# Optimization experiments

Hardware: AMD Instinct MI355X
Metric: run time of the kernel (lower is better)

Reference implementation:

```python
import jax, jax.numpy as jnp
import numpy as np
from jax import lax

MAX_LEN = 40
SOS_ID = 2
VOCAB, EMB, HID, CTX = 32000, 512, 1024, 64
H2 = HID // 2
B, S = 256, 128


def gru_cell(x, h, wih, whh, bih, bhh):
    # PyTorch GRU equations: gates ordered (r, z, n)
    gx = x @ wih.T + bih
    gh = h @ whh.T + bhh
    rx, zx, nx = jnp.split(gx, 3, axis=-1)
    rh, zh, nh = jnp.split(gh, 3, axis=-1)
    r = jax.nn.sigmoid(rx + rh)
    z = jax.nn.sigmoid(zx + zh)
    n = jnp.tanh(nx + r * nh)
    return (1.0 - z) * n + z * h


def setup_inputs() -> dict:
    key = jax.random.key(0)
    ks = jax.random.split(key, 16)
    sd = 0.02
    emb_table = jax.random.normal(ks[0], (VOCAB, EMB), jnp.float32) * sd
    emb_table = emb_table.at[0].set(0.0)  # padding_idx=0
    def w(k, shape):
        return jax.random.normal(k, shape, jnp.float32) * sd
    inp = {
        "input_ids": jax.random.randint(ks[1], (B, S), 0, VOCAB),
        "context_vec": jax.random.normal(ks[2], (B, CTX), jnp.float32),
        "emb_table": emb_table,
        # encoder fwd direction
        "enc_wih_f": w(ks[3], (3 * H2, EMB)),
        "enc_whh_f": w(ks[4], (3 * H2, H2)),
        "enc_bih_f": w(ks[5], (3 * H2,)),
        "enc_bhh_f": w(ks[6], (3 * H2,)),
        # encoder bwd direction
        "enc_wih_b": w(ks[7], (3 * H2, EMB)),
        "enc_whh_b": w(ks[8], (3 * H2, H2)),
        "enc_bih_b": w(ks[9], (3 * H2,)),
        "enc_bhh_b": w(ks[10], (3 * H2,)),
        # decoder GRU: input = emb + hidden + context
        "dec_wih": w(ks[11], (3 * HID, EMB + HID + CTX)),
        "dec_whh": w(ks[12], (3 * HID, HID)),
        "dec_bih": w(ks[13], (3 * HID,)),
        "dec_bhh": w(ks[14], (3 * HID,)),
        "wout": w(ks[15], (VOCAB, HID)),
        "bout": jnp.zeros((VOCAB,), jnp.float32),
    }
    return inp


def reference(input_ids, context_vec, emb_table,
              enc_wih_f, enc_whh_f, enc_bih_f, enc_bhh_f,
              enc_wih_b, enc_whh_b, enc_bih_b, enc_bhh_b,
              dec_wih, dec_whh, dec_bih, dec_bhh, wout, bout):
    b = input_ids.shape[0]
    emb = emb_table[input_ids]                      # [B,S,E]
    emb_t = jnp.swapaxes(emb, 0, 1)                 # [S,B,E]

    def enc_f(h, x):
        return gru_cell(x, h, enc_wih_f, enc_whh_f, enc_bih_f, enc_bhh_f), None

    def enc_b(h, x):
        return gru_cell(x, h, enc_wih_b, enc_whh_b, enc_bih_b, enc_bhh_b), None

    h0 = jnp.zeros((b, H2), emb.dtype)
    hf, _ = lax.scan(enc_f, h0, emb_t)
    hb, _ = lax.scan(enc_b, h0, emb_t[::-1])
    # replicate torch's h_n.view(batch, -1) on a (2,B,H2) tensor (contiguous reshape)
    encoder_ctx = jnp.stack([hf, hb], axis=0).reshape(b, HID)   # [B,HID]

    ctx = jnp.concatenate([encoder_ctx, context_vec], axis=-1)  # [B,HID+CTX]
    h_dec0 = jnp.zeros((b, HID), emb.dtype)
    prev0 = jnp.full((b,), SOS_ID, dtype=jnp.int32)

    def dec_step(carry, _):
        h, prev = carry
        x = jnp.concatenate([emb_table[prev], ctx], axis=-1)
        h = gru_cell(x, h, dec_wih, dec_whh, dec_bih, dec_bhh)
        logits = h @ wout.T + bout                  # [B,V]
        probs = jax.nn.softmax(logits, axis=-1)
        nxt = jnp.argmax(probs, axis=-1).astype(jnp.int32)
        sel = jnp.take_along_axis(probs, nxt[:, None], axis=1)[:, 0]
        lp = jnp.log(sel + 1e-12)
        return (h, nxt), (nxt, lp)

    (_, _), (toks, lps) = lax.scan(dec_step, (h_dec0, prev0), None, length=MAX_LEN)
    return toks.T, lps.T   # [B,MAX_LEN] tokens, [B,MAX_LEN] log-probs
```

## Files before the change

kernel.cpp:

```cpp
#include <hip/hip_runtime.h>
#include <hip/hip_bf16.h>
#include <math.h>

#define B_    256
#define S_    128
#define EMB_  512
#define H2_   512
#define HID_  1024
#define CTX_  64
#define VOC_  32000
#define TMAX_ 40
#define SOS_  2

typedef unsigned short u16;
typedef __attribute__((ext_vector_type(8))) short short8;
typedef __attribute__((ext_vector_type(4))) float f32x4;

__device__ __forceinline__ float4 ld4(const float* p) {
    return *reinterpret_cast<const float4*>(p);
}
__device__ __forceinline__ float sigmoidf_(float x) { return 1.f / (1.f + expf(-x)); }
__device__ __forceinline__ u16 f2bf(float x) {
    union { float f; unsigned int u; } v; v.f = x;
    unsigned int r = v.u + 0x7FFFu + ((v.u >> 16) & 1u);
    return (u16)(r >> 16);
}
__device__ __forceinline__ unsigned pk2(float a, float b) {
    float2 t; t.x = a; t.y = b;
    __hip_bfloat162 h = __float22bfloat162_rn(t);
    return *reinterpret_cast<unsigned*>(&h);
}
__device__ __forceinline__ void merge_top2(float& v1, int& i1, float& v2, int& i2,
                                           float ov1, int oi1, float ov2, int oi2)
{
    if (ov1 > v1 || (ov1 == v1 && oi1 < i1)) {
        float tv = v1; int ti = i1;
        v1 = ov1; i1 = oi1;
        if (ov2 > tv || (ov2 == tv && oi2 < ti)) { v2 = ov2; i2 = oi2; }
        else                                     { v2 = tv;  i2 = ti;  }
    } else {
        if (ov1 > v2 || (ov1 == v2 && oi1 < i2)) { v2 = ov1; i2 = oi1; }
    }
}

template<int BM, int BN, int TM, int TN, int AMODE, int BGATHER, int BIASM>
__launch_bounds__(256)
__global__ void gemm_nt(const float* __restrict__ Ap,
                        const int*   __restrict__ ids,
                        const float* __restrict__ Ex,
                        const float* __restrict__ Bp, int ldb, int bofs,
                        const float* __restrict__ bias,
                        const float* __restrict__ addsrc,
                        float* __restrict__ Cp, int ldc,
                        int lda, int K, int s_base, int sdir)
{
    constexpr int BK = 32;
    __shared__ float As[BK][BM + 4];
    __shared__ float Bs[BK][BN + 4];
    const int t  = threadIdx.x;
    const int tx = t & 15, ty = t >> 4;
    const int m_base = blockIdx.y * BM;
    const int n_base = blockIdx.x * BN;

    float acc[TM][TN];
#pragma unroll
    for (int i = 0; i < TM; ++i)
#pragma unroll
        for (int j = 0; j < TN; ++j) acc[i][j] = 0.f;

    constexpr int A_PER = BM * BK / 4 / 256;
    constexpr int B_PER = BN * BK / 4 / 256;

    for (int k0 = 0; k0 < K; k0 += BK) {
#pragma unroll
        for (int j = 0; j < A_PER; ++j) {
            int f   = t + j * 256;
            int row = f >> 3;
            int kk  = (f & 7) << 2;
            int m   = m_base + row;
            float4 v;
            if constexpr (AMODE == 0) {
                v = ld4(Ap + (size_t)m * lda + k0 + kk);
            } else if constexpr (AMODE == 3) {
                int id = ids[m];
                v = ld4(Ex + (size_t)id * EMB_ + k0 + kk);
            } else {
                int k = k0 + kk;
                if (k < HID_) v = ld4(Ap + (size_t)m * HID_ + k);
                else          v = ld4(Ex + (size_t)m * CTX_ + (k - HID_));
            }
            As[kk + 0][row] = v.x; As[kk + 1][row] = v.y;
            As[kk + 2][row] = v.z; As[kk + 3][row] = v.w;
        }
#pragma unroll
        for (int j = 0; j < B_PER; ++j) {
            int f   = t + j * 256;
            int row = f >> 3;
            int kk  = (f & 7) << 2;
            float4 v;
            if constexpr (BGATHER == 1) {
                int n = n_base + row;
                int s = n >> 8, b = n & 255;
                int id = ids[b * S_ + s_base + sdir * s];
                v = ld4(Ex + (size_t)id * EMB_ + k0 + kk);
            } else {
                v = ld4(Bp + (size_t)(n_base + row) * ldb + bofs + k0 + kk);
            }
            Bs[kk + 0][row] = v.x; Bs[kk + 1][row] = v.y;
            Bs[kk + 2][row] = v.z; Bs[kk + 3][row] = v.w;
        }
        __syncthreads();
#pragma unroll
        for (int kk = 0; kk < BK; ++kk) {
            float a[TM], b[TN];
            *(float4*)&a[0] = ld4(&As[kk][ty * TM]);
            if constexpr (TM == 8) *(float4*)&a[4] = ld4(&As[kk][ty * TM + 4]);
            *(float4*)&b[0] = ld4(&Bs[kk][tx * TN]);
            if constexpr (TN == 8) *(float4*)&b[4] = ld4(&Bs[kk][tx * TN + 4]);
#pragma unroll
            for (int i = 0; i < TM; ++i)
#pragma unroll
                for (int j = 0; j < TN; ++j) acc[i][j] += a[i] * b[j];
        }
        __syncthreads();
    }
#pragma unroll
    for (int i = 0; i < TM; ++i) {
        int m = m_base + ty * TM + i;
#pragma unroll
        for (int j = 0; j < TN; ++j) {
            int n = n_base + tx * TN + j;
            float v = acc[i][j];
            if (bias) v += BIASM ? bias[m] : bias[n];
            if (addsrc) v += addsrc[(size_t)m * ldc + n];
            Cp[(size_t)m * ldc + n] = v;
        }
    }
}

__global__ void whh_trans(const float* __restrict__ whh_f, const float* __restrict__ whh_b,
                          float* __restrict__ whhU_f, float* __restrict__ whhU_b)
{
    int idx = blockIdx.x * 256 + threadIdx.x;
    const float* src = blockIdx.y ? whh_b : whh_f;
    float*       dst = blockIdx.y ? whhU_b : whhU_f;
    int k  = idx / 1536;
    int rem = idx - k * 1536;
    int g  = rem >> 9;
    int u  = rem & 511;
    dst[idx] = src[(size_t)(g * 512 + u) * 512 + k];
}

__global__ void wbf_conv(const float* __restrict__ wout, unsigned* __restrict__ wbf, int npairs)
{
    int idx = blockIdx.x * 256 + threadIdx.x;
    if (idx >= npairs) return;
    float2 v = *reinterpret_cast<const float2*>(wout + (size_t)idx * 2);
    wbf[idx] = pk2(v.x, v.y);
}

union EncSM {
    struct { float hbuf[2][512][4]; } rec;
    struct { float As[32][132]; float Bs[32][132]; } gx;
};

__launch_bounds__(512)
__global__ void enc_fused(const float* __restrict__ grec_f, const float* __restrict__ grec_b,
                          float* __restrict__ gout_f, float* __restrict__ gout_b,
                          const float* __restrict__ whhU_f, const float* __restrict__ whhU_b,
                          const float* __restrict__ bhh_f, const float* __restrict__ bhh_b,
                          const float* __restrict__ wih_f, const float* __restrict__ wih_b,
                          const float* __restrict__ bih_f, const float* __restrict__ bih_b,
                          const int* __restrict__ ids, const float* __restrict__ emb,
                          float* __restrict__ hT, int do_rec, int gx_chunk, int nsteps)
{
    __shared__ __align__(16) EncSM sm;
    const int t = threadIdx.x;
    const int idx = blockIdx.x;
    const int grp = idx & 15;

    if (grp >= 8) {
        if (gx_chunk < 0) return;
        const int g = (idx >> 4) * 8 + (grp - 8);
        const int dz  = g >= 192;
        const int t192 = dz ? g - 192 : g;
        const int m_base = (t192 & 15) * 128;
        const int n_base = (t192 >> 4) * 128;
        const float* W    = dz ? wih_b : wih_f;
        const float* bias = dz ? bih_b : bih_f;
        float*       Cp   = dz ? gout_b : gout_f;
        const int s_base  = dz ? (127 - 8 * gx_chunk) : (8 * gx_chunk);
        const int sdir    = dz ? -1 : 1;
        const int tx = t & 31, ty = t >> 5;

        float acc[8][4];
#pragma unroll
        for (int i = 0; i < 8; ++i)
#pragma unroll
            for (int j = 0; j < 4; ++j) acc[i][j] = 0.f;

        for (int k0 = 0; k0 < 512; k0 += 32) {
#pragma unroll
            for (int j = 0; j < 2; ++j) {
                int f   = t + j * 512;
                int row = f >> 3;
                int kk  = (f & 7) << 2;
                int m   = m_base + row;
                int s   = m >> 8, b = m & 255;
                int id  = ids[b * S_ + s_base + sdir * s];
                float4 v = ld4(emb + (size_t)id * EMB_ + k0 + kk);
                sm.gx.As[kk + 0][row] = v.x; sm.gx.As[kk + 1][row] = v.y;
                sm.gx.As[kk + 2][row] = v.z; sm.gx.As[kk + 3][row] = v.w;
                float4 wv = ld4(W + (size_t)(n_base + row) * 512 + k0 + kk);
                sm.gx.Bs[kk + 0][row] = wv.x; sm.gx.Bs[kk + 1][row] = wv.y;
                sm.gx.Bs[kk + 2][row] = wv.z; sm.gx.Bs[kk + 3][row] = wv.w;
            }
            __syncthreads();
#pragma unroll
            for (int kk = 0; kk < 32; ++kk) {
                float a[8], b[4];
                *(float4*)&a[0] = ld4(&sm.gx.As[kk][ty * 8]);
                *(float4*)&a[4] = ld4(&sm.gx.As[kk][ty * 8 + 4]);
                *(float4*)&b[0] = ld4(&sm.gx.Bs[kk][tx * 4]);
#pragma unroll
                for (int i = 0; i < 8; ++i)
#pragma unroll
                    for (int j = 0; j < 4; ++j) acc[i][j] += a[i] * b[j];
            }
            __syncthreads();
        }
#pragma unroll
        for (int i = 0; i < 8; ++i) {
            int m = m_base + ty * 8 + i;
#pragma unroll
            for (int j = 0; j < 4; ++j) {
                int n = n_base + tx * 4 + j;
                Cp[(size_t)m * 1536 + n] = acc[i][j] + bias[n];
            }
        }
        return;
    }

    if (idx >= 256 || !do_rec) return;
    const int xcd = idx & 7;
    const int dir = xcd >> 2;
    const int local = (idx >> 4) * 4 + (xcd & 3);
    const int r0 = local * 4;
    const float* gx  = dir ? grec_b : grec_f;
    const float* whx = dir ? whhU_b : whhU_f;
    const float* bhh = dir ? bhh_b : bhh_f;
    float* hTd = hT + (size_t)dir * (256 * 512);

    const int u = t;

#pragma unroll
    for (int r = 0; r < 4; ++r)
        sm.rec.hbuf[0][u][r] = hTd[(size_t)(r0 + r) * 512 + u];
    const float bh0 = bhh[u], bh1 = bhh[512 + u], bh2 = bhh[1024 + u];
    __syncthreads();

    for (int st = 0; st < nsteps; ++st) {
        const int cur = st & 1, nxt = cur ^ 1;

        float gx0[4], gx1[4], gx2[4];
#pragma unroll
        for (int r = 0; r < 4; ++r) {
            size_t base = (size_t)((st << 8) + r0 + r) * 1536 + u;
            gx0[r] = gx[base];
            gx1[r] = gx[base + 512];
            gx2[r] = gx[base + 1024];
        }

        float acc0[4] = {0.f,0.f,0.f,0.f};
        float acc1[4] = {0.f,0.f,0.f,0.f};
        float acc2[4] = {0.f,0.f,0.f,0.f};
        const float* wp = whx + u;
#pragma unroll 8
        for (int kk = 0; kk < 512; ++kk) {
            float4 hv = *(const float4*)&sm.rec.hbuf[cur][kk][0];
            float w0 = wp[0], w1 = wp[512], w2 = wp[1024];
            const float* hvp = (const float*)&hv;
#pragma unroll
            for (int r = 0; r < 4; ++r) {
                acc0[r] += w0 * hvp[r];
                acc1[r] += w1 * hvp[r];
                acc2[r] += w2 * hvp[r];
            }
            wp += 1536;
        }

#pragma unroll
        for (int r = 0; r < 4; ++r) {
            float hold = sm.rec.hbuf[cur][u][r];
            float rg = sigmoidf_(gx0[r] + acc0[r] + bh0);
            float zg = sigmoidf_(gx1[r] + acc1[r] + bh1);
            float ng = tanhf(gx2[r] + rg * (acc2[r] + bh2));
            sm.rec.hbuf[nxt][u][r] = (1.f - zg) * ng + zg * hold;
        }
        __syncthreads();
    }

    const int lb = nsteps & 1;
#pragma unroll
    for (int r = 0; r < 4; ++r)
        hTd[(size_t)(r0 + r) * 512 + u] = sm.rec.hbuf[lb][u][r];
}

__global__ void zerof(float* __restrict__ p, int n)
{
    int i = blockIdx.x * 256 + threadIdx.x;
    if (i < n) p[i] = 0.f;
}

__global__ void init_dec(float* __restrict__ hdec, u16* __restrict__ hbf, int* __restrict__ prev)
{
    int i = blockIdx.x * 256 + threadIdx.x;
    hdec[i] = 0.f; hbf[i] = 0;
    if (i < B_) prev[i] = SOS_;
}

__global__ void hcat_build(const float* __restrict__ hT, float* __restrict__ hcat)
{
    int idx = blockIdx.x * 256 + threadIdx.x;
    int b = idx >> 10, k = idx & 1023;
    int d = b >> 7;
    int rr = ((2 * b) & 255) + (k >> 9);
    int kk = k & 511;
    hcat[idx] = hT[(size_t)d * 131072 + (size_t)rr * 512 + kk];
}

__launch_bounds__(256)
__global__ void dec_gemm2(const float* __restrict__ hdec, const int* __restrict__ prev,
                          const float* __restrict__ emb,
                          const float* __restrict__ dwhh, const float* __restrict__ dwih,
                          const float* __restrict__ dbhh, const float* __restrict__ gctx,
                          float* __restrict__ ghbuf, float* __restrict__ gibuf)
{
    constexpr int BK = 32;
    __shared__ float As[BK][68];
    __shared__ float Bs[BK][68];
    const int t  = threadIdx.x;
    const int tx = t & 15, ty = t >> 4;
    const bool isH = blockIdx.y < 4;
    const int m_base = (isH ? blockIdx.y : (blockIdx.y - 4)) * 64;
    const int n_base = blockIdx.x * 64;
    const int K   = isH ? 1024 : 512;
    const float* Bp = isH ? dwhh : dwih;
    const int ldb  = isH ? 1024 : 1600;
    float* Cp = isH ? ghbuf : gibuf;

    float acc[4][4];
#pragma unroll
    for (int i = 0; i < 4; ++i)
#pragma unroll
        for (int j = 0; j < 4; ++j) acc[i][j] = 0.f;

    for (int k0 = 0; k0 < K; k0 += BK) {
#pragma unroll
        for (int j = 0; j < 2; ++j) {
            int f   = t + j * 256;
            int row = f >> 3;
            int kk  = (f & 7) << 2;
            int m   = m_base + row;
            float4 v;
            if (isH) v = ld4(hdec + (size_t)m * HID_ + k0 + kk);
            else     v = ld4(emb + (size_t)prev[m] * EMB_ + k0 + kk);
            As[kk + 0][row] = v.x; As[kk + 1][row] = v.y;
            As[kk + 2][row] = v.z; As[kk + 3][row] = v.w;
            float4 w = ld4(Bp + (size_t)(n_base + row) * ldb + k0 + kk);
            Bs[kk + 0][row] = w.x; Bs[kk + 1][row] = w.y;
            Bs[kk + 2][row] = w.z; Bs[kk + 3][row] = w.w;
        }
        __syncthreads();
#pragma unroll
        for (int kk = 0; kk < BK; ++kk) {
            float a[4], b[4];
            *(float4*)&a[0] = ld4(&As[kk][ty * 4]);
            *(float4*)&b[0] = ld4(&Bs[kk][tx * 4]);
#pragma unroll
            for (int i = 0; i < 4; ++i)
#pragma unroll
                for (int j = 0; j < 4; ++j) acc[i][j] += a[i] * b[j];
        }
        __syncthreads();
    }
#pragma unroll
    for (int i = 0; i < 4; ++i) {
        int m = m_base + ty * 4 + i;
#pragma unroll
        for (int j = 0; j < 4; ++j) {
            int n = n_base + tx * 4 + j;
            float v = acc[i][j];
            if (isH) v += dbhh[n];
            else     v += gctx[(size_t)m * 3072 + n];
            Cp[(size_t)m * 3072 + n] = v;
        }
    }
}

__launch_bounds__(256)
__global__ void dec_gi(const int* __restrict__ prev, const float* __restrict__ emb,
                       const float* __restrict__ dwih, const float* __restrict__ gctx,
                       float* __restrict__ gibuf)
{
    constexpr int BK = 32;
    __shared__ float As[BK][68];
    __shared__ float Bs[BK][68];
    const int t  = threadIdx.x;
    const int tx = t & 15, ty = t >> 4;
    const int m_base = blockIdx.y * 64;
    const int n_base = blockIdx.x * 64;

    float acc[4][4];
#pragma unroll
    for (int i = 0; i < 4; ++i)
#pragma unroll
        for (int j = 0; j < 4; ++j) acc[i][j] = 0.f;

    for (int k0 = 0; k0 < 512; k0 += BK) {
#pragma unroll
        for (int j = 0; j < 2; ++j) {
            int f   = t + j * 256;
            int row = f >> 3;
            int kk  = (f & 7) << 2;
            int m   = m_base + row;
            float4 v = ld4(emb + (size_t)prev[m] * EMB_ + k0 + kk);
            As[kk + 0][row] = v.x; As[kk + 1][row] = v.y;
            As[kk + 2][row] = v.z; As[kk + 3][row] = v.w;
            float4 w = ld4(dwih + (size_t)(n_base + row) * 1600 + k0 + kk);
            Bs[kk + 0][row] = w.x; Bs[kk + 1][row] = w.y;
            Bs[kk + 2][row] = w.z; Bs[kk + 3][row] = w.w;
        }
        __syncthreads();
#pragma unroll
        for (int kk = 0; kk < BK; ++kk) {
            float a[4], b[4];
            *(float4*)&a[0] = ld4(&As[kk][ty * 4]);
            *(float4*)&b[0] = ld4(&Bs[kk][tx * 4]);
#pragma unroll
            for (int i = 0; i < 4; ++i)
#pragma unroll
                for (int j = 0; j < 4; ++j) acc[i][j] += a[i] * b[j];
        }
        __syncthreads();
    }
#pragma unroll
    for (int i = 0; i < 4; ++i) {
        int m = m_base + ty * 4 + i;
#pragma unroll
        for (int j = 0; j < 4; ++j) {
            int n = n_base + tx * 4 + j;
            gibuf[(size_t)m * 3072 + n] = acc[i][j] + gctx[(size_t)m * 3072 + n];
        }
    }
}

__global__ void dec_combine(const float* __restrict__ gi, const float* __restrict__ gh,
                            float* __restrict__ hdec, u16* __restrict__ hbf)
{
    int idx = blockIdx.x * 256 + threadIdx.x;
    int b = idx >> 10, u = idx & 1023;
    size_t gb = (size_t)b * 3072;
    float r = sigmoidf_(gi[gb + u]            + gh[gb + u]);
    float z = sigmoidf_(gi[gb + HID_ + u]     + gh[gb + HID_ + u]);
    float n = tanhf    (gi[gb + 2 * HID_ + u] + r * gh[gb + 2 * HID_ + u]);
    float v = (1.f - z) * n + z * hdec[idx];
    hdec[idx] = v;
    hbf[idx] = f2bf(v);
}

union DecSM {
    struct { u16 As[256][72]; u16 Bs[128][72]; } lg;
    struct { float As[32][68]; float Bs[32][68]; } gh;
};

__launch_bounds__(512)
__global__ void dec_lh(const u16* __restrict__ A, const float* __restrict__ Wf,
                       const u16* __restrict__ Wbf, int wbfRows,
                       const float* __restrict__ bias,
                       float* __restrict__ pmax, float* __restrict__ psum,
                       float* __restrict__ ptv, int* __restrict__ pti,
                       const float* __restrict__ hdec, const float* __restrict__ dwhh,
                       const float* __restrict__ dbhh, float* __restrict__ ghbuf,
                       int doGh)
{
    __shared__ __align__(16) DecSM sm;
    const int t = threadIdx.x;

    if (blockIdx.y == 1) {
        if (!doGh || blockIdx.x >= 192) return;
        const int g  = blockIdx.x;
        const int m0 = (g / 48) * 64;
        const int n0 = (g % 48) * 64;
        const int tx = t & 15, ty = t >> 4;

        float acc[2][4];
#pragma unroll
        for (int i = 0; i < 2; ++i)
#pragma unroll
            for (int j = 0; j < 4; ++j) acc[i][j] = 0.f;

        for (int k0 = 0; k0 < 1024; k0 += 32) {
            {
                int row = t >> 3;
                int kk  = (t & 7) << 2;
                float4 v = ld4(hdec + (size_t)(m0 + row) * HID_ + k0 + kk);
                sm.gh.As[kk + 0][row] = v.x; sm.gh.As[kk + 1][row] = v.y;
                sm.gh.As[kk + 2][row] = v.z; sm.gh.As[kk + 3][row] = v.w;
                float4 w = ld4(dwhh + (size_t)(n0 + row) * 1024 + k0 + kk);
                sm.gh.Bs[kk + 0][row] = w.x; sm.gh.Bs[kk + 1][row] = w.y;
                sm.gh.Bs[kk + 2][row] = w.z; sm.gh.Bs[kk + 3][row] = w.w;
            }
            __syncthreads();
#pragma unroll
            for (int kk = 0; kk < 32; ++kk) {
                float2 a = *(const float2*)&sm.gh.As[kk][ty * 2];
                float b[4];
                *(float4*)&b[0] = ld4(&sm.gh.Bs[kk][tx * 4]);
#pragma unroll
                for (int j = 0; j < 4; ++j) {
                    acc[0][j] += a.x * b[j];
                    acc[1][j] += a.y * b[j];
                }
            }
            __syncthreads();
        }
#pragma unroll
        for (int i = 0; i < 2; ++i) {
            int m = m0 + ty * 2 + i;
#pragma unroll
            for (int j = 0; j < 4; ++j) {
                int n = n0 + tx * 4 + j;
                ghbuf[(size_t)m * 3072 + n] = acc[i][j] + dbhh[n];
            }
        }
        return;
    }

    const int lane = t & 63, wave = t >> 6;
    const int wm = (wave & 3) * 64, wn = (wave >> 2) * 64;
    const int n0 = blockIdx.x * 128;
    f32x4 acc[4][4];
#pragma unroll
    for (int i = 0; i < 4; ++i)
#pragma unroll
        for (int j = 0; j < 4; ++j) acc[i][j] = (f32x4){0.f, 0.f, 0.f, 0.f};
    const int arow = t >> 1, aoff = (t & 1) * 32;
    const int brow = t >> 2, boff = (t & 3) * 16;
    const bool useBf = (n0 + brow) < wbfRows;

    for (int k0 = 0; k0 < 1024; k0 += 64) {
#pragma unroll
        for (int q = 0; q < 4; ++q) {
            *(uint4*)&sm.lg.As[arow][aoff + q * 8] =
                *(const uint4*)(A + (size_t)arow * 1024 + k0 + aoff + q * 8);
        }
        if (useBf) {
            const u16* wr = Wbf + (size_t)(n0 + brow) * 1024 + k0 + boff;
            *(uint4*)&sm.lg.Bs[brow][boff]     = *(const uint4*)(wr);
            *(uint4*)&sm.lg.Bs[brow][boff + 8] = *(const uint4*)(wr + 8);
        } else {
            const float* wr = Wf + (size_t)(n0 + brow) * 1024 + k0 + boff;
#pragma unroll
            for (int q = 0; q < 2; ++q) {
                float4 x = ld4(wr + q * 8);
                float4 y = ld4(wr + q * 8 + 4);
                uint4 o;
                o.x = pk2(x.x, x.y); o.y = pk2(x.z, x.w);
                o.z = pk2(y.x, y.y); o.w = pk2(y.z, y.w);
                *(uint4*)&sm.lg.Bs[brow][boff + q * 8] = o;
            }
        }
        __syncthreads();
#pragma unroll
        for (int s = 0; s < 2; ++s) {
            short8 a[4], b[4];
            int j0 = s * 32 + (lane >> 4) * 8;
#pragma unroll
            for (int i = 0; i < 4; ++i) {
                a[i] = *(const short8*)&sm.lg.As[wm + i * 16 + (lane & 15)][j0];
                b[i] = *(const short8*)&sm.lg.Bs[wn + i * 16 + (lane & 15)][j0];
            }
#pragma unroll
            for (int i = 0; i < 4; ++i)
#pragma unroll
                for (int j = 0; j < 4; ++j)
                    acc[i][j] = __builtin_amdgcn_mfma_f32_16x16x32_bf16(a[i], b[j], acc[i][j], 0, 0, 0);
        }
        __syncthreads();
    }

    const int htile = blockIdx.x * 2 + (wn >> 6);
    float bn[4]; int jx[4];
#pragma unroll
    for (int j = 0; j < 4; ++j) { jx[j] = n0 + wn + j * 16 + (lane & 15); bn[j] = bias[jx[j]]; }
#pragma unroll
    for (int i = 0; i < 4; ++i) {
#pragma unroll
        for (int rr = 0; rr < 4; ++rr) {
            float v[4];
#pragma unroll
            for (int j = 0; j < 4; ++j) v[j] = acc[i][j][rr] + bn[j];
            float v1 = v[0], v2 = -3.4e38f; int i1 = jx[0], i2 = 0x7fffffff;
#pragma unroll
            for (int j = 1; j < 4; ++j) {
                if (v[j] > v1)      { v2 = v1; i2 = i1; v1 = v[j]; i1 = jx[j]; }
                else if (v[j] > v2) { v2 = v[j]; i2 = jx[j]; }
            }
#pragma unroll
            for (int mask = 1; mask <= 8; mask <<= 1) {
                float ov1 = __shfl_xor(v1, mask), ov2 = __shfl_xor(v2, mask);
                int   oi1 = __shfl_xor(i1, mask), oi2 = __shfl_xor(i2, mask);
                merge_top2(v1, i1, v2, i2, ov1, oi1, ov2, oi2);
            }
            float rmax = v1;
            float s = 0.f;
#pragma unroll
            for (int j = 0; j < 4; ++j) s += expf(v[j] - rmax);
#pragma unroll
            for (int mask = 1; mask <= 8; mask <<= 1) s += __shfl_xor(s, mask);
            if ((lane & 15) == 0) {
                int row = wm + i * 16 + (lane >> 4) * 4 + rr;
                size_t base = (size_t)row * 500 + htile;
                pmax[base] = rmax; psum[base] = s;
                ptv[base * 2] = v1; ptv[base * 2 + 1] = v2;
                pti[base * 2] = i1; pti[base * 2 + 1] = i2;
            }
        }
    }
}

__launch_bounds__(256)
__global__ void dec_reduce(const float* __restrict__ pmax, const float* __restrict__ psum,
                           const float* __restrict__ ptv, const int* __restrict__ pti,
                           const float* __restrict__ hdec, const float* __restrict__ wout,
                           const float* __restrict__ bout,
                           float* __restrict__ out, int* __restrict__ prev, int tstep)
{
    __shared__ float sv[256]; __shared__ int sti[256]; __shared__ int ssl[256];
    __shared__ float cvv[1000]; __shared__ int cii[1000];
    __shared__ float c8v[8]; __shared__ int c8i[8]; __shared__ float c8e[8];
    const int b = blockIdx.x, tid = threadIdx.x;
    const float* pm = pmax + (size_t)b * 500;
    const float* ps = psum + (size_t)b * 500;

    float m = -3.4e38f;
    for (int i = tid; i < 500; i += 256) m = fmaxf(m, pm[i]);
    sv[tid] = m; __syncthreads();
    for (int off = 128; off; off >>= 1) { if (tid < off) sv[tid] = fmaxf(sv[tid], sv[tid + off]); __syncthreads(); }
    float gmax = sv[0]; __syncthreads();

    float s = 0.f;
    for (int i = tid; i < 500; i += 256) s += ps[i] * expf(pm[i] - gmax);
    sv[tid] = s; __syncthreads();
    for (int off = 128; off; off >>= 1) { if (tid < off) sv[tid] += sv[tid + off]; __syncthreads(); }
    float gsum = sv[0]; __syncthreads();

    for (int i = tid; i < 1000; i += 256) { cvv[i] = ptv[(size_t)b * 1000 + i]; cii[i] = pti[(size_t)b * 1000 + i]; }
    __syncthreads();

    for (int c = 0; c < 8; ++c) {
        float bv = -3.4e38f; int bi = 0x7fffffff, bs = 0;
        for (int i = tid; i < 1000; i += 256) {
            float v = cvv[i]; int ix = cii[i];
            if (v > bv || (v == bv && ix < bi)) { bv = v; bi = ix; bs = i; }
        }
        sv[tid] = bv; sti[tid] = bi; ssl[tid] = bs; __syncthreads();
        for (int off = 128; off; off >>= 1) {
            if (tid < off) {
                if (sv[tid + off] > sv[tid] ||
                    (sv[tid + off] == sv[tid] && sti[tid + off] < sti[tid])) {
                    sv[tid] = sv[tid + off]; sti[tid] = sti[tid + off]; ssl[tid] = ssl[tid + off];
                }
            }
            __syncthreads();
        }
        if (tid == 0) { c8v[c] = sv[0]; c8i[c] = sti[0]; cvv[ssl[0]] = -3.4e38f; }
        __syncthreads();
    }

    {
        int lane = tid & 63, wv = tid >> 6;
        const float* hr = hdec + (size_t)b * HID_;
        for (int c = wv; c < 8; c += 4) {
            const float* wr = wout + (size_t)c8i[c] * HID_;
            float a = 0.f;
            for (int k = lane * 4; k < HID_; k += 256) {
                float4 x = ld4(hr + k), y = ld4(wr + k);
                a += x.x * y.x + x.y * y.y + x.z * y.z + x.w * y.w;
            }
#pragma unroll
            for (int off = 32; off; off >>= 1) a += __shfl_down(a, off);
            if (lane == 0) c8e[c] = a + bout[c8i[c]];
        }
    }
    __syncthreads();

    if (tid == 0) {
        float bv = c8e[0]; int bi = c8i[0]; float av = c8v[0];
        for (int c = 1; c < 8; ++c)
            if (c8e[c] > bv || (c8e[c] == bv && c8i[c] < bi)) { bv = c8e[c]; bi = c8i[c]; av = c8v[c]; }
        float p = expf(av - gmax) / gsum;
        float lp = logf(p + 1e-12f);
        out[(size_t)b * TMAX_ + tstep] = (float)bi;
        out[B_ * TMAX_ + (size_t)b * TMAX_ + tstep] = lp;
        prev[b] = bi;
    }
}

extern "C" void kernel_launch(void* const* d_in, const int* in_sizes, int n_in,
                              void* d_out, int out_size, void* d_ws, size_t ws_size,
                              hipStream_t stream)
{
    const int*   ids   = (const int*)  d_in[0];
    const float* cvec  = (const float*)d_in[1];
    const float* emb   = (const float*)d_in[2];
    const float* wih_f = (const float*)d_in[3];
    const float* whh_f = (const float*)d_in[4];
    const float* bih_f = (const float*)d_in[5];
    const float* bhh_f = (const float*)d_in[6];
    const float* wih_b = (const float*)d_in[7];
    const float* whh_b = (const float*)d_in[8];
    const float* bih_b = (const float*)d_in[9];
    const float* bhh_b = (const float*)d_in[10];
    const float* dwih  = (const float*)d_in[11];
    const float* dwhh  = (const float*)d_in[12];
    const float* dbih  = (const float*)d_in[13];
    const float* dbhh  = (const float*)d_in[14];
    const float* wout  = (const float*)d_in[15];
    const float* bout  = (const float*)d_in[16];
    float* out = (float*)d_out;

    float* w      = (float*)d_ws;
    float* buf0_f = w;
    float* buf0_b = w + 3145728;
    float* buf1_f = w + 6291456;
    float* buf1_b = w + 9437184;
    float* hT     = w + 12582912;
    float* hcat   = w + 12845056;
    float* hdec   = w + 13107200;
    float* gctx   = w + 13369344;
    u16*   hdecb  = (u16*)(w + 14155776);
    int*   prev   = (int*)(w + 14286848);
    float* whhU_f = w + 14287104;
    float* whhU_b = w + 15073536;
    u16*   wbf_big = (u16*)(w + 15859968);
    const int big_ws = (ws_size >= (size_t)(15859968 + 16384000) * 4);
    float* gibuf  = w;
    float* ghbuf  = w + 786432;
    float* pmax   = w + 1572864;
    float* psum   = w + 1700864;
    float* ptv    = w + 1828864;
    int*   pti    = (int*)(w + 2084864);
    u16*   wbf_part = (u16*)(w + 2340864);
    const int wbfRows = big_ws ? VOC_ : 20992;
    u16* wbfPtr = big_ws ? wbf_big : wbf_part;

    zerof<<<1024, 256, 0, stream>>>(hT, 262144);
    init_dec<<<1024, 256, 0, stream>>>(hdec, hdecb, prev);
    whh_trans<<<dim3(3072, 2), 256, 0, stream>>>(whh_f, whh_b, whhU_f, whhU_b);

    enc_fused<<<768, 512, 0, stream>>>(
        buf0_f, buf0_b, buf0_f, buf0_b, whhU_f, whhU_b, bhh_f, bhh_b,
        wih_f, wih_b, bih_f, bih_b, ids, emb, hT, 0, 0, 8);
    for (int c = 1; c < 16; ++c) {
        float* rf = ((c - 1) & 1) ? buf1_f : buf0_f;
        float* rb = ((c - 1) & 1) ? buf1_b : buf0_b;
        float* of = (c & 1) ? buf1_f : buf0_f;
        float* ob = (c & 1) ? buf1_b : buf0_b;
        enc_fused<<<768, 512, 0, stream>>>(
            rf, rb, of, ob, whhU_f, whhU_b, bhh_f, bhh_b,
            wih_f, wih_b, bih_f, bih_b, ids, emb, hT, 1, c, 8);
    }
    enc_fused<<<768, 512, 0, stream>>>(
        buf1_f, buf1_b, buf1_f, buf1_b, whhU_f, whhU_b, bhh_f, bhh_b,
        wih_f, wih_b, bih_f, bih_b, ids, emb, hT, 1, -1, 8);

    hcat_build<<<1024, 256, 0, stream>>>(hT, hcat);

    {
        int npairs = wbfRows * 512;
        wbf_conv<<<(npairs + 255) / 256, 256, 0, stream>>>(wout, (unsigned*)wbfPtr, npairs);
    }

    gemm_nt<64, 64, 4, 4, 2, 0, 0><<<dim3(48, 4), 256, 0, stream>>>(
        hcat, nullptr, cvec, dwih, 1600, 512, dbih, nullptr,
        gctx, 3072, 1024, 1088, 0, 0);

    dec_gemm2<<<dim3(48, 8), 256, 0, stream>>>(
        hdec, prev, emb, dwhh, dwih, dbhh, gctx, ghbuf, gibuf);
    dec_combine<<<1024, 256, 0, stream>>>(gibuf, ghbuf, hdec, hdecb);
    for (int t = 0; t < TMAX_; ++t) {
        dec_lh<<<dim3(250, 2), 512, 0, stream>>>(
            hdecb, wout, wbfPtr, wbfRows, bout,
            pmax, psum, ptv, pti, hdec, dwhh, dbhh, ghbuf, (t < TMAX_ - 1));
        dec_reduce<<<256, 256, 0, stream>>>(pmax, psum, ptv, pti,
                                            hdec, wout, bout, out, prev, t);
        if (t < TMAX_ - 1) {
            dec_gi<<<dim3(48, 4), 256, 0, stream>>>(prev, emb, dwih, gctx, gibuf);
            dec_combine<<<1024, 256, 0, stream>>>(gibuf, ghbuf, hdec, hdecb);
        }
    }
}
```

Before: 9.556 ms.

## Fuse decoder input GEMM with GRU combine and widen encoder recurrence rows

The decoder input-gate GEMM and the GRU combine kernel are merged into one kernel. It uses a transposed, gate-interleaved copy of the embedding part of dec_wih, so each block holds all three gates for its hidden units and can apply the nonlinearity in place, without writing and rereading gibuf. The encoder recurrence blocks now each process 8 batch rows instead of 4, which halves the number of recurrence blocks and gives more of the grid to the input-projection GEMM tiles. The cost is more registers per recurrence thread and a one-time transpose. The transposed buffer also reuses workspace that previously held whhU_f after the encoder has finished.

```diff
diff --git a/kernel.cpp b/kernel.cpp
--- a/kernel.cpp
+++ b/kernel.cpp
@@ -151,6 +151,15 @@
     dst[idx] = src[(size_t)(g * 512 + u) * 512 + k];
 }
 
+__global__ void dwi_trans(const float* __restrict__ dwih, float* __restrict__ dwiX)
+{
+    int idx = blockIdx.x * 256 + threadIdx.x;
+    if (idx >= 1572864) return;
+    int c = idx >> 9, k = idx & 511;
+    int u = c / 3, g = c - u * 3;
+    dwiX[idx] = dwih[(size_t)(g * 1024 + u) * 1600 + k];
+}
+
 __global__ void wbf_conv(const float* __restrict__ wout, unsigned* __restrict__ wbf, int npairs)
 {
     int idx = blockIdx.x * 256 + threadIdx.x;
@@ -160,7 +169,7 @@
 }
 
 union EncSM {
-    struct { float hbuf[2][512][4]; } rec;
+    struct { float hbuf[2][512][8]; } rec;
     struct { float As[32][132]; float Bs[32][132]; } gx;
 };
 
@@ -179,9 +188,11 @@
     const int idx = blockIdx.x;
     const int grp = idx & 15;
 
-    if (grp >= 8) {
+    if (grp >= 4) {
         if (gx_chunk < 0) return;
-        const int g = (idx >> 4) * 8 + (grp - 8);
+        int g;
+        if (idx < 256) g = (idx >> 4) * 12 + (grp - 4);
+        else           g = 192 + ((idx - 256) >> 4) * 12 + (grp - 4);
         const int dz  = g >= 192;
         const int t192 = dz ? g - 192 : g;
         const int m_base = (t192 & 15) * 128;
@@ -242,10 +253,9 @@
     }
 
     if (idx >= 256 || !do_rec) return;
-    const int xcd = idx & 7;
-    const int dir = xcd >> 2;
-    const int local = (idx >> 4) * 4 + (xcd & 3);
-    const int r0 = local * 4;
+    const int dir = grp >> 1;
+    const int local = (idx >> 4) * 2 + (grp & 1);
+    const int r0 = local * 8;
     const float* gx  = dir ? grec_b : grec_f;
     const float* whx = dir ? whhU_b : whhU_f;
     const float* bhh = dir ? bhh_b : bhh_f;
@@ -254,7 +264,7 @@
     const int u = t;
 
 #pragma unroll
-    for (int r = 0; r < 4; ++r)
+    for (int r = 0; r < 8; ++r)
         sm.rec.hbuf[0][u][r] = hTd[(size_t)(r0 + r) * 512 + u];
     const float bh0 = bhh[u], bh1 = bhh[512 + u], bh2 = bhh[1024 + u];
     __syncthreads();
@@ -262,35 +272,37 @@
     for (int st = 0; st < nsteps; ++st) {
         const int cur = st & 1, nxt = cur ^ 1;
 
-        float gx0[4], gx1[4], gx2[4];
-#pragma unroll
-        for (int r = 0; r < 4; ++r) {
+        float gx0[8], gx1[8], gx2[8];
+#pragma unroll
+        for (int r = 0; r < 8; ++r) {
             size_t base = (size_t)((st << 8) + r0 + r) * 1536 + u;
             gx0[r] = gx[base];
             gx1[r] = gx[base + 512];
             gx2[r] = gx[base + 1024];
         }
 
-        float acc0[4] = {0.f,0.f,0.f,0.f};
-        float acc1[4] = {0.f,0.f,0.f,0.f};
-        float acc2[4] = {0.f,0.f,0.f,0.f};
+        float acc0[8], acc1[8], acc2[8];
+#pragma unroll
+        for (int r = 0; r < 8; ++r) { acc0[r] = 0.f; acc1[r] = 0.f; acc2[r] = 0.f; }
         const float* wp = whx + u;
-#pragma unroll 8
+#pragma unroll 4
         for (int kk = 0; kk < 512; ++kk) {
-            float4 hv = *(const float4*)&sm.rec.hbuf[cur][kk][0];
+            float4 h0 = *(const float4*)&sm.rec.hbuf[cur][kk][0];
+            float4 h1 = *(const float4*)&sm.rec.hbuf[cur][kk][4];
             float w0 = wp[0], w1 = wp[512], w2 = wp[1024];
-            const float* hvp = (const float*)&hv;
-#pragma unroll
-            for (int r = 0; r < 4; ++r) {
-                acc0[r] += w0 * hvp[r];
-                acc1[r] += w1 * hvp[r];
-                acc2[r] += w2 * hvp[r];
+            float hv[8];
+            *(float4*)&hv[0] = h0; *(float4*)&hv[4] = h1;
+#pragma unroll
+            for (int r = 0; r < 8; ++r) {
+                acc0[r] += w0 * hv[r];
+                acc1[r] += w1 * hv[r];
+                acc2[r] += w2 * hv[r];
             }
             wp += 1536;
         }
 
 #pragma unroll
-        for (int r = 0; r < 4; ++r) {
+        for (int r = 0; r < 8; ++r) {
             float hold = sm.rec.hbuf[cur][u][r];
             float rg = sigmoidf_(gx0[r] + acc0[r] + bh0);
             float zg = sigmoidf_(gx1[r] + acc1[r] + bh1);
@@ -302,7 +314,7 @@
 
     const int lb = nsteps & 1;
 #pragma unroll
-    for (int r = 0; r < 4; ++r)
+    for (int r = 0; r < 8; ++r)
         hTd[(size_t)(r0 + r) * 512 + u] = sm.rec.hbuf[lb][u][r];
 }
 
@@ -398,63 +410,6 @@
     }
 }
 
-__launch_bounds__(256)
-__global__ void dec_gi(const int* __restrict__ prev, const float* __restrict__ emb,
-                       const float* __restrict__ dwih, const float* __restrict__ gctx,
-                       float* __restrict__ gibuf)
-{
-    constexpr int BK = 32;
-    __shared__ float As[BK][68];
-    __shared__ float Bs[BK][68];
-    const int t  = threadIdx.x;
-    const int tx = t & 15, ty = t >> 4;
-    const int m_base = blockIdx.y * 64;
-    const int n_base = blockIdx.x * 64;
-
-    float acc[4][4];
-#pragma unroll
-    for (int i = 0; i < 4; ++i)
-#pragma unroll
-        for (int j = 0; j < 4; ++j) acc[i][j] = 0.f;
-
-    for (int k0 = 0; k0 < 512; k0 += BK) {
-#pragma unroll
-        for (int j = 0; j < 2; ++j) {
-            int f   = t + j * 256;
-            int row = f >> 3;
-            int kk  = (f & 7) << 2;
-            int m   = m_base + row;
-            float4 v = ld4(emb + (size_t)prev[m] * EMB_ + k0 + kk);
-            As[kk + 0][row] = v.x; As[kk + 1][row] = v.y;
-            As[kk + 2][row] = v.z; As[kk + 3][row] = v.w;
-            float4 w = ld4(dwih + (size_t)(n_base + row) * 1600 + k0 + kk);
-            Bs[kk + 0][row] = w.x; Bs[kk + 1][row] = w.y;
-            Bs[kk + 2][row] = w.z; Bs[kk + 3][row] = w.w;
-        }
-        __syncthreads();
-#pragma unroll
-        for (int kk = 0; kk < BK; ++kk) {
-            float a[4], b[4];
-            *(float4*)&a[0] = ld4(&As[kk][ty * 4]);
-            *(float4*)&b[0] = ld4(&Bs[kk][tx * 4]);
-#pragma unroll
-            for (int i = 0; i < 4; ++i)
-#pragma unroll
-                for (int j = 0; j < 4; ++j) acc[i][j] += a[i] * b[j];
-        }
-        __syncthreads();
-    }
-#pragma unroll
-    for (int i = 0; i < 4; ++i) {
-        int m = m_base + ty * 4 + i;
-#pragma unroll
-        for (int j = 0; j < 4; ++j) {
-            int n = n_base + tx * 4 + j;
-            gibuf[(size_t)m * 3072 + n] = acc[i][j] + gctx[(size_t)m * 3072 + n];
-        }
-    }
-}
-
 __global__ void dec_combine(const float* __restrict__ gi, const float* __restrict__ gh,
                             float* __restrict__ hdec, u16* __restrict__ hbf)
 {
@@ -467,6 +422,84 @@
     float v = (1.f - z) * n + z * hdec[idx];
     hdec[idx] = v;
     hbf[idx] = f2bf(v);
+}
+
+__launch_bounds__(256)
+__global__ void dec_gic(const int* __restrict__ prev, const float* __restrict__ emb,
+                        const float* __restrict__ dwiX, const float* __restrict__ gctx,
+                        const float* __restrict__ ghbuf,
+                        float* __restrict__ hdec, u16* __restrict__ hbf)
+{
+    constexpr int BK = 32;
+    __shared__ float As[BK][36];
+    __shared__ float Bs[BK][100];
+    const int t  = threadIdx.x;
+    const int tx = t & 15, ty = t >> 4;
+    const int m0 = blockIdx.y * 32;
+    const int c0 = blockIdx.x * 96;
+    const int u0 = blockIdx.x * 32;
+
+    float acc[2][6];
+#pragma unroll
+    for (int i = 0; i < 2; ++i)
+#pragma unroll
+        for (int j = 0; j < 6; ++j) acc[i][j] = 0.f;
+
+    for (int k0 = 0; k0 < 512; k0 += BK) {
+        {
+            int row = t >> 3;
+            int kk  = (t & 7) << 2;
+            float4 v = ld4(emb + (size_t)prev[m0 + row] * EMB_ + k0 + kk);
+            As[kk + 0][row] = v.x; As[kk + 1][row] = v.y;
+            As[kk + 2][row] = v.z; As[kk + 3][row] = v.w;
+        }
+#pragma unroll
+        for (int j = 0; j < 3; ++j) {
+            int f   = t + j * 256;
+            int row = f >> 3;
+            int kk  = (f & 7) << 2;
+            float4 v = ld4(dwiX + (size_t)(c0 + row) * 512 + k0 + kk);
+            Bs[kk + 0][row] = v.x; Bs[kk + 1][row] = v.y;
+            Bs[kk + 2][row] = v.z; Bs[kk + 3][row] = v.w;
+        }
+        __syncthreads();
+#pragma unroll
+        for (int kk = 0; kk < BK; ++kk) {
+            float2 a = *(const float2*)&As[kk][ty * 2];
+            float b[6];
+            *(float2*)&b[0] = *(const float2*)&Bs[kk][tx * 6];
+            *(float2*)&b[2] = *(const float2*)&Bs[kk][tx * 6 + 2];
+            *(float2*)&b[4] = *(const float2*)&Bs[kk][tx * 6 + 4];
+#pragma unroll
+            for (int j = 0; j < 6; ++j) {
+                acc[0][j] += a.x * b[j];
+                acc[1][j] += a.y * b[j];
+            }
+        }
+        __syncthreads();
+    }
+
+#pragma unroll
+    for (int i = 0; i < 2; ++i) {
+        int m = m0 + ty * 2 + i;
+#pragma unroll
+        for (int ul = 0; ul < 2; ++ul) {
+            int u = u0 + tx * 2 + ul;
+            float gir = acc[i][ul * 3 + 0] + gctx[(size_t)m * 3072 + u];
+            float giz = acc[i][ul * 3 + 1] + gctx[(size_t)m * 3072 + 1024 + u];
+            float gin = acc[i][ul * 3 + 2] + gctx[(size_t)m * 3072 + 2048 + u];
+            float ghr = ghbuf[(size_t)m * 3072 + u];
+            float ghz = ghbuf[(size_t)m * 3072 + 1024 + u];
+            float ghn = ghbuf[(size_t)m * 3072 + 2048 + u];
+            float r = sigmoidf_(gir + ghr);
+            float z = sigmoidf_(giz + ghz);
+            float n = tanhf(gin + r * ghn);
+            float hold = hdec[(size_t)m * HID_ + u];
+            float v = (1.f - z) * n + z * hold;
+            hdec[(size_t)m * HID_ + u] = v;
+            hbf[(size_t)m * HID_ + u] = f2bf(v);
+        }
+    }
 }
 
 union DecSM {
@@ -753,6 +786,7 @@
     float* ptv    = w + 1828864;
     int*   pti    = (int*)(w + 2084864);
     u16*   wbf_part = (u16*)(w + 2340864);
+    float* dwiX   = w + 14287104;
     const int wbfRows = big_ws ? VOC_ : 20992;
     u16* wbfPtr = big_ws ? wbf_big : wbf_part;
 
@@ -760,7 +794,7 @@
     init_dec<<<1024, 256, 0, stream>>>(hdec, hdecb, prev);
     whh_trans<<<dim3(3072, 2), 256, 0, stream>>>(whh_f, whh_b, whhU_f, whhU_b);
 
-    enc_fused<<<768, 512, 0, stream>>>(
+    enc_fused<<<512, 512, 0, stream>>>(
         buf0_f, buf0_b, buf0_f, buf0_b, whhU_f, whhU_b, bhh_f, bhh_b,
         wih_f, wih_b, bih_f, bih_b, ids, emb, hT, 0, 0, 8);
     for (int c = 1; c < 16; ++c) {
@@ -768,11 +802,11 @@
         float* rb = ((c - 1) & 1) ? buf1_b : buf0_b;
         float* of = (c & 1) ? buf1_f : buf0_f;
         float* ob = (c & 1) ? buf1_b : buf0_b;
-        enc_fused<<<768, 512, 0, stream>>>(
+        enc_fused<<<512, 512, 0, stream>>>(
             rf, rb, of, ob, whhU_f, whhU_b, bhh_f, bhh_b,
             wih_f, wih_b, bih_f, bih_b, ids, emb, hT, 1, c, 8);
     }
-    enc_fused<<<768, 512, 0, stream>>>(
+    enc_fused<<<512, 512, 0, stream>>>(
         buf1_f, buf1_b, buf1_f, buf1_b, whhU_f, whhU_b, bhh_f, bhh_b,
         wih_f, wih_b, bih_f, bih_b, ids, emb, hT, 1, -1, 8);
 
@@ -782,6 +816,7 @@
         int npairs = wbfRows * 512;
         wbf_conv<<<(npairs + 255) / 256, 256, 0, stream>>>(wout, (unsigned*)wbfPtr, npairs);
     }
+    dwi_trans<<<6144, 256, 0, stream>>>(dwih, dwiX);
 
     gemm_nt<64, 64, 4, 4, 2, 0, 0><<<dim3(48, 4), 256, 0, stream>>>(
         hcat, nullptr, cvec, dwih, 1600, 512, dbih, nullptr,
@@ -797,8 +832,8 @@
         dec_reduce<<<256, 256, 0, stream>>>(pmax, psum, ptv, pti,
                                             hdec, wout, bout, out, prev, t);
         if (t < TMAX_ - 1) {
-            dec_gi<<<dim3(48, 4), 256, 0, stream>>>(prev, emb, dwih, gctx, gibuf);
-            dec_combine<<<1024, 256, 0, stream>>>(gibuf, ghbuf, hdec, hdecb);
-        }
-    }
-}
+            dec_gic<<<dim3(32, 8), 256, 0, stream>>>(
+                prev, emb, dwiX, gctx, ghbuf, hdec, hdecb);
+        }
+    }
+}
```

Measured after the change: 12.59 ms. +31.8%, slower.
